# Kernel tuning notes

Hardware: AMD Instinct MI355X
Metric: run time of the kernel (lower is better)

## Reference

```python
import jax, jax.numpy as jnp
import numpy as np


def _gcn_conv(X, src, dst, norm, W, n_nodes):
    # gather + normalized aggregate (SpMM) then dense linear (GEMM)
    msg = X[src] * norm[:, None]                       # [E, F]
    agg = jax.ops.segment_sum(msg, dst, num_segments=n_nodes)  # [N, F]
    return agg @ W                                     # [N, F_out]


def setup_inputs() -> dict:
    key = jax.random.key(0)
    k1, k2, k3, k4, k5 = jax.random.split(key, 5)
    N, E, D_IN, D_HID, D_OUT = 50000, 800000, 128, 128, 64
    X = jax.random.normal(k1, (N, D_IN), dtype=jnp.float32)
    edge_index = jax.random.randint(k2, (2, E), 0, N, dtype=jnp.int64)
    s = 1.0 / np.sqrt(D_IN)
    W1 = jax.random.normal(k3, (D_IN, D_HID), dtype=jnp.float32) * s
    W2 = jax.random.normal(k4, (D_HID, D_HID), dtype=jnp.float32) * s
    W3 = jax.random.normal(k5, (D_HID, D_OUT), dtype=jnp.float32) * s
    return {"X": X, "edge_index": edge_index, "W1": W1, "W2": W2, "W3": W3}


def reference(X, edge_index, W1, W2, W3):
    n_nodes = X.shape[0]
    src, dst = edge_index[0], edge_index[1]
    # symmetric degree normalization D^-1/2 A D^-1/2 (degrees from edge list)
    ones = jnp.ones(src.shape[0], dtype=X.dtype)
    deg = jax.ops.segment_sum(ones, dst, num_segments=n_nodes)
    deg = jnp.maximum(deg, 1.0)
    dinv = jax.lax.rsqrt(deg)
    norm = dinv[src] * dinv[dst]                       # [E]
    h = jax.nn.relu(_gcn_conv(X, src, dst, norm, W1, n_nodes))
    h = jax.nn.relu(_gcn_conv(h, src, dst, norm, W2, n_nodes))
    h = jax.nn.relu(_gcn_conv(h, src, dst, norm, W3, n_nodes))
    return jax.nn.softmax(h, axis=-1)
```

## Files before the change

kernel.cpp:

```cpp
#include <hip/hip_runtime.h>
#include <hip/hip_bf16.h>

typedef __attribute__((ext_vector_type(8))) short short8;
typedef __attribute__((ext_vector_type(4))) short short4v;
typedef __attribute__((ext_vector_type(4))) float f32x4;

static inline size_t ws_align(size_t x) { return (x + 511) & ~((size_t)511); }

static __device__ inline unsigned short f2bf(float f) {
    __hip_bfloat16 h = __float2bfloat16(f);
    return __builtin_bit_cast(unsigned short, h);
}

static __device__ inline float bf2f(unsigned short u) {
    unsigned int x = ((unsigned int)u) << 16;
    return __builtin_bit_cast(float, x);
}


template <int FOUT>
static __device__ inline void gemm64_body(const void* __restrict__ Araw, int a_fp32,
                                          const void* __restrict__ Wraw, int w_fp32,
                                          unsigned short* __restrict__ out,
                                          int N, int blk) {
    constexpr int K = 128;
    constexpr int NT = FOUT / 16;
    constexpr int LDB = K + 8;
    constexpr int LDA = K + 8;
    __shared__ __align__(16) unsigned short bt[FOUT * LDB];
    __shared__ __align__(16) unsigned short atile[64 * LDA];

    const int tid = threadIdx.x;
    const int base = blk * 64;

    constexpr int TOT4 = K * FOUT / 4;
    if (w_fp32) {
        const float* Wf = (const float*)Wraw;
        for (int i = tid; i < TOT4; i += 256) {
            int idx = i * 4;
            int k = idx / FOUT;
            int n = idx & (FOUT - 1);
            float4 v = *(const float4*)(const void*)(Wf + idx);
            bt[(n + 0) * LDB + k] = f2bf(v.x);
            bt[(n + 1) * LDB + k] = f2bf(v.y);
            bt[(n + 2) * LDB + k] = f2bf(v.z);
            bt[(n + 3) * LDB + k] = f2bf(v.w);
        }
    } else {
        const unsigned short* Ws = (const unsigned short*)Wraw;
        for (int i = tid; i < TOT4; i += 256) {
            int idx = i * 4;
            int k = idx / FOUT;
            int n = idx & (FOUT - 1);
            short4v v = *(const short4v*)(const void*)(Ws + idx);
#pragma unroll
            for (int j = 0; j < 4; j++) bt[(n + j) * LDB + k] = ((const unsigned short*)&v)[j];
        }
    }

    if (a_fp32) {
        const float* Af = (const float*)Araw;
#pragma unroll
        for (int i = 0; i < 8; i++) {
            int e4 = i * 256 + tid;
            int elem = e4 * 4;
            int r = elem >> 7;
            int c = elem & 127;
            int srow = base + r;
            if (srow > N - 1) srow = N - 1;
            float4 v = *(const float4*)(const void*)(Af + (size_t)srow * K + c);
            unsigned short* dst = &atile[r * LDA + c];
            dst[0] = f2bf(v.x); dst[1] = f2bf(v.y); dst[2] = f2bf(v.z); dst[3] = f2bf(v.w);
        }
    } else {
        const unsigned short* Ab = (const unsigned short*)Araw;
#pragma unroll
        for (int i = 0; i < 4; i++) {
            int e8 = i * 256 + tid;
            int elem = e8 * 8;
            int r = elem >> 7;
            int c = elem & 127;
            int srow = base + r;
            if (srow > N - 1) srow = N - 1;
            *(short8*)(void*)(&atile[r * LDA + c]) =
                *(const short8*)(const void*)(Ab + (size_t)srow * K + c);
        }
    }

    __syncthreads();

    const int wave = tid >> 6;
    const int lane = tid & 63;
    const int quad = lane >> 4;
    const int r16 = lane & 15;

    short8 afrag[4];
#pragma unroll
    for (int kk = 0; kk < 4; kk++)
        afrag[kk] = *(const short8*)(const void*)(&atile[(wave * 16 + r16) * LDA + kk * 32 + quad * 8]);

    f32x4 acc[NT];
#pragma unroll
    for (int nt = 0; nt < NT; nt++) acc[nt] = (f32x4){0.f, 0.f, 0.f, 0.f};

#pragma unroll
    for (int kk = 0; kk < 4; kk++) {
#pragma unroll
        for (int nt = 0; nt < NT; nt++) {
            short8 b = *(const short8*)(const void*)(&bt[(nt * 16 + r16) * LDB + kk * 32 + quad * 8]);
            acc[nt] = __builtin_amdgcn_mfma_f32_16x16x32_bf16(afrag[kk], b, acc[nt], 0, 0, 0);
        }
    }

#pragma unroll
    for (int nt = 0; nt < NT; nt++) {
#pragma unroll
        for (int r = 0; r < 4; r++) {
            float v = acc[nt][r];
            float o = __shfl_xor(v, 1, 64);
            int row = base + wave * 16 + quad * 4 + r;
            if (((lane & 1) == 0) && row < N) {
                __hip_bfloat162 pk;
                pk.x = __float2bfloat16(v);
                pk.y = __float2bfloat16(o);
                *(__hip_bfloat162*)(out + (size_t)row * FOUT + nt * 16 + r16) = pk;
            }
        }
    }
}


__global__ __launch_bounds__(256) void gemm1_hist_kernel(const void* __restrict__ Xraw,
                                                         const unsigned short* __restrict__ w1s,
                                                         const int* __restrict__ ei,
                                                         int* __restrict__ counts,
                                                         int* __restrict__ loff,
                                                         int* __restrict__ flags,
                                                         unsigned short* __restrict__ out,
                                                         int N, int E, int gblocks) {
    const int tid = threadIdx.x;
    const int lane = tid & 63;

    unsigned ew = (w1s[2 * lane] >> 7) & 0xFF;
    unsigned long long m1 = __ballot(ew >= 100 && ew <= 130);
    const int in_fp32 = (__popcll(m1) < 48) ? 1 : 0;

    if (blockIdx.x >= gblocks) {
        unsigned long long m2 = __ballot(((const unsigned int*)ei)[2 * lane + 1] == 0u);
        const int ei64 = (__popcll(m2) >= 48) ? 1 : 0;
        if (blockIdx.x == gblocks && tid == 0) {
            flags[0] = in_fp32;
            flags[1] = ei64;
        }
        int e = (blockIdx.x - gblocks) * 256 + tid;
        if (e < E) {
            int d = ei64 ? ei[2 * (size_t)E + 2 * e] : ei[(size_t)E + e];
            loff[e] = atomicAdd(&counts[d], 1);
        }
        return;
    }

    gemm64_body<128>(Xraw, in_fp32, (const void*)w1s, in_fp32, out, N, blockIdx.x);
}


template <int FOUT>
__global__ __launch_bounds__(256) void gemm_kernel(const void* __restrict__ Araw,
                                                   const void* __restrict__ Wraw,
                                                   const int* __restrict__ flags,
                                                   unsigned short* __restrict__ out, int N) {
    gemm64_body<FOUT>(Araw, 0, Wraw, flags[0], out, N, blockIdx.x);
}


__global__ __launch_bounds__(256) void alloc_kernel(const int* __restrict__ counts,
                                                    float* __restrict__ dinv,
                                                    int* __restrict__ rowptr,
                                                    int* __restrict__ total, int N) {
    int n = blockIdx.x * blockDim.x + threadIdx.x;
    int lane = threadIdx.x & 63;
    int c = (n < N) ? counts[n] : 0;
    if (n < N) {
        int d = (c < 1) ? 1 : c;
        dinv[n] = rsqrtf((float)d);
    }
    int incl = c;
#pragma unroll
    for (int off = 1; off < 64; off <<= 1) {
        int v = __shfl_up(incl, off, 64);
        if (lane >= off) incl += v;
    }
    int wavetot = __shfl(incl, 63, 64);
    int base = 0;
    if (lane == 0) base = atomicAdd(total, wavetot);
    base = __shfl(base, 0, 64);
    if (n < N) rowptr[n] = base + incl - c;
}

__global__ void fill_kernel(const int* __restrict__ ei, const int* __restrict__ flags,
                            const float* __restrict__ dinv, const int* __restrict__ rowptr,
                            const int* __restrict__ loff, int2* __restrict__ edgedat, int E) {
    int e = blockIdx.x * blockDim.x + threadIdx.x;
    if (e < E) {
        int s, d;
        if (flags[1]) {
            s = ei[2 * e];
            d = ei[2 * (size_t)E + 2 * e];
        } else {
            s = ei[e];
            d = ei[(size_t)E + e];
        }
        int pos = rowptr[d] + loff[e];
        float wt = dinv[s] * dinv[d];
        edgedat[pos] = make_int2(s, __float_as_int(wt));
    }
}


__global__ __launch_bounds__(256) void spmm128_kernel(const int2* __restrict__ edgedat,
                                                      const int* __restrict__ rowptr,
                                                      const int* __restrict__ counts,
                                                      const unsigned short* __restrict__ Hin,
                                                      unsigned short* __restrict__ Hout, int N) {
    int wid = (blockIdx.x * 256 + threadIdx.x) >> 6;
    if (wid >= N) return;
    int lane = threadIdx.x & 63;
    int grp = lane >> 4;
    int gl = lane & 15;
    int n = __builtin_amdgcn_readfirstlane(wid);
    int start = __builtin_amdgcn_readfirstlane(rowptr[n]);
    int len = __builtin_amdgcn_readfirstlane(counts[n]);
    const int2* ep = edgedat + start;

    float acc[8];
#pragma unroll
    for (int u = 0; u < 8; u++) acc[u] = 0.f;

    int j = 0;
    for (; j + 8 <= len; j += 8) {
        int2 e0 = ep[j + grp];
        int2 e1 = ep[j + 4 + grp];
        short8 h0 = *(const short8*)(const void*)(Hin + (size_t)e0.x * 128 + gl * 8);
        short8 h1 = *(const short8*)(const void*)(Hin + (size_t)e1.x * 128 + gl * 8);
        float w0 = __int_as_float(e0.y);
        float w1 = __int_as_float(e1.y);
#pragma unroll
        for (int u = 0; u < 8; u++) acc[u] += w0 * bf2f((unsigned short)h0[u]);
#pragma unroll
        for (int u = 0; u < 8; u++) acc[u] += w1 * bf2f((unsigned short)h1[u]);
    }
    for (; j + 4 <= len; j += 4) {
        int2 e = ep[j + grp];
        short8 h = *(const short8*)(const void*)(Hin + (size_t)e.x * 128 + gl * 8);
        float w = __int_as_float(e.y);
#pragma unroll
        for (int u = 0; u < 8; u++) acc[u] += w * bf2f((unsigned short)h[u]);
    }
    int rem = len - j;
    if (grp < rem) {
        int2 e = ep[j + grp];
        short8 h = *(const short8*)(const void*)(Hin + (size_t)e.x * 128 + gl * 8);
        float w = __int_as_float(e.y);
#pragma unroll
        for (int u = 0; u < 8; u++) acc[u] += w * bf2f((unsigned short)h[u]);
    }

#pragma unroll
    for (int u = 0; u < 8; u++) {
        acc[u] += __shfl_xor(acc[u], 16, 64);
        acc[u] += __shfl_xor(acc[u], 32, 64);
    }

    if (grp == 0) {
        short8 o;
#pragma unroll
        for (int u = 0; u < 8; u++) o[u] = (short)f2bf(fmaxf(acc[u], 0.f));
        *(short8*)(void*)(Hout + (size_t)n * 128 + gl * 8) = o;
    }
}


__global__ __launch_bounds__(256) void spmm64_softmax_kernel(const int2* __restrict__ edgedat,
                                                             const int* __restrict__ rowptr,
                                                             const int* __restrict__ counts,
                                                             const unsigned short* __restrict__ Hin,
                                                             const int* __restrict__ flags,
                                                             void* __restrict__ Out, int N) {
    int wid = (blockIdx.x * 256 + threadIdx.x) >> 6;
    if (wid >= N) return;
    int lane = threadIdx.x & 63;
    int grp = lane >> 3;
    int gl = lane & 7;
    int n = __builtin_amdgcn_readfirstlane(wid);
    int start = __builtin_amdgcn_readfirstlane(rowptr[n]);
    int len = __builtin_amdgcn_readfirstlane(counts[n]);
    const int2* ep = edgedat + start;

    float acc[8];
#pragma unroll
    for (int u = 0; u < 8; u++) acc[u] = 0.f;

    int j = 0;
    for (; j + 16 <= len; j += 16) {
        int2 e0 = ep[j + grp];
        int2 e1 = ep[j + 8 + grp];
        short8 h0 = *(const short8*)(const void*)(Hin + (size_t)e0.x * 64 + gl * 8);
        short8 h1 = *(const short8*)(const void*)(Hin + (size_t)e1.x * 64 + gl * 8);
        float w0 = __int_as_float(e0.y);
        float w1 = __int_as_float(e1.y);
#pragma unroll
        for (int u = 0; u < 8; u++) acc[u] += w0 * bf2f((unsigned short)h0[u]);
#pragma unroll
        for (int u = 0; u < 8; u++) acc[u] += w1 * bf2f((unsigned short)h1[u]);
    }
    for (; j + 8 <= len; j += 8) {
        int2 e = ep[j + grp];
        short8 h = *(const short8*)(const void*)(Hin + (size_t)e.x * 64 + gl * 8);
        float w = __int_as_float(e.y);
#pragma unroll
        for (int u = 0; u < 8; u++) acc[u] += w * bf2f((unsigned short)h[u]);
    }
    int rem = len - j;
    if (grp < rem) {
        int2 e = ep[j + grp];
        short8 h = *(const short8*)(const void*)(Hin + (size_t)e.x * 64 + gl * 8);
        float w = __int_as_float(e.y);
#pragma unroll
        for (int u = 0; u < 8; u++) acc[u] += w * bf2f((unsigned short)h[u]);
    }

#pragma unroll
    for (int u = 0; u < 8; u++) {
        acc[u] += __shfl_xor(acc[u], 8, 64);
        acc[u] += __shfl_xor(acc[u], 16, 64);
        acc[u] += __shfl_xor(acc[u], 32, 64);
    }

#pragma unroll
    for (int u = 0; u < 8; u++) acc[u] = fmaxf(acc[u], 0.f);

    float m = acc[0];
#pragma unroll
    for (int u = 1; u < 8; u++) m = fmaxf(m, acc[u]);
#pragma unroll
    for (int off = 1; off < 8; off <<= 1) m = fmaxf(m, __shfl_xor(m, off, 64));

    float ex[8];
    float s = 0.f;
#pragma unroll
    for (int u = 0; u < 8; u++) {
        ex[u] = __expf(acc[u] - m);
        s += ex[u];
    }
#pragma unroll
    for (int off = 1; off < 8; off <<= 1) s += __shfl_xor(s, off, 64);
    float inv = 1.0f / s;

    if (grp == 0) {
        if (flags[0]) {
            float* op = (float*)Out + (size_t)n * 64 + gl * 8;
            float4 v0, v1;
            v0.x = ex[0] * inv; v0.y = ex[1] * inv; v0.z = ex[2] * inv; v0.w = ex[3] * inv;
            v1.x = ex[4] * inv; v1.y = ex[5] * inv; v1.z = ex[6] * inv; v1.w = ex[7] * inv;
            *(float4*)(void*)op = v0;
            *(float4*)(void*)(op + 4) = v1;
        } else {
            short8 o;
#pragma unroll
            for (int u = 0; u < 8; u++) o[u] = (short)f2bf(ex[u] * inv);
            *(short8*)(void*)((unsigned short*)Out + (size_t)n * 64 + gl * 8) = o;
        }
    }
}


extern "C" void kernel_launch(void* const* d_in, const int* in_sizes, int n_in,
                              void* d_out, int out_size, void* d_ws, size_t ws_size,
                              hipStream_t stream) {
    const void* X  = d_in[0];
    const int*  ei = (const int*)d_in[1];
    const void* W1 = d_in[2];
    const void* W2 = d_in[3];
    const void* W3 = d_in[4];

    const int N = in_sizes[0] / 128;
    const int E = in_sizes[1] / 2;

    char* ws = (char*)d_ws;
    size_t off = 0;
    int* counts = (int*)(ws + off);   off += ws_align((size_t)N * 4);
    int* total  = (int*)(ws + off);   off += ws_align(64);
    const size_t zero_bytes = off;
    int* flags    = (int*)(ws + off);   off += ws_align(64);
    int* rowptr   = (int*)(ws + off);   off += ws_align((size_t)N * 4);
    float* dinv   = (float*)(ws + off); off += ws_align((size_t)N * 4);
    int* loff     = (int*)(ws + off);   off += ws_align((size_t)E * 4);
    int2* edgedat = (int2*)(ws + off);  off += ws_align((size_t)E * 8);
    unsigned short* HA = (unsigned short*)(ws + off); off += ws_align((size_t)N * 128 * 2);
    unsigned short* HB = (unsigned short*)(ws + off); off += ws_align((size_t)N * 128 * 2);

    hipMemsetAsync(d_ws, 0, zero_bytes, stream);

    const int gblocks = (N + 63) / 64;
    const int hblocks = (E + 255) / 256;
    const int sblocks = (N * 64 + 255) / 256;

    gemm1_hist_kernel<<<gblocks + hblocks, 256, 0, stream>>>(
        X, (const unsigned short*)W1, ei, counts, loff, flags, HA, N, E, gblocks);
    alloc_kernel<<<(N + 255) / 256, 256, 0, stream>>>(counts, dinv, rowptr, total, N);
    fill_kernel<<<hblocks, 256, 0, stream>>>(ei, flags, dinv, rowptr, loff, edgedat, E);

    spmm128_kernel<<<sblocks, 256, 0, stream>>>(edgedat, rowptr, counts, HA, HB, N);
    gemm_kernel<128><<<gblocks, 256, 0, stream>>>(HB, W2, flags, HA, N);
    spmm128_kernel<<<sblocks, 256, 0, stream>>>(edgedat, rowptr, counts, HA, HB, N);
    gemm_kernel<64><<<gblocks, 256, 0, stream>>>(HB, W3, flags, HA, N);
    spmm64_softmax_kernel<<<sblocks, 256, 0, stream>>>(edgedat, rowptr, counts, HA, flags, d_out, N);
}
```

Measured before the change: 276.5 us.

## Load GEMM A fragments directly from global and use 128-row 512-thread blocks

The dense GEMM stage now has each wave load its A-operand MFMA fragments straight from global memory into registers, dropping the shared-memory A tile and its staging pass. Blocks grow to 512 threads covering 128 rows, so each staged copy of the transposed weight matrix is reused across twice as many rows. The histogram part of the fused first kernel also moves to 512-thread blocks. The risks are strided, less coalesced global reads for A and lower occupancy from the larger blocks.

```diff
diff --git a/kernel.cpp b/kernel.cpp
--- a/kernel.cpp
+++ b/kernel.cpp
@@ -19,24 +19,22 @@
 
 
 template <int FOUT>
-static __device__ inline void gemm64_body(const void* __restrict__ Araw, int a_fp32,
-                                          const void* __restrict__ Wraw, int w_fp32,
-                                          unsigned short* __restrict__ out,
-                                          int N, int blk) {
+static __device__ inline void gemm128_body(const void* __restrict__ Araw, int a_fp32,
+                                           const void* __restrict__ Wraw, int w_fp32,
+                                           unsigned short* __restrict__ out,
+                                           int N, int blk) {
     constexpr int K = 128;
     constexpr int NT = FOUT / 16;
     constexpr int LDB = K + 8;
-    constexpr int LDA = K + 8;
     __shared__ __align__(16) unsigned short bt[FOUT * LDB];
-    __shared__ __align__(16) unsigned short atile[64 * LDA];
 
     const int tid = threadIdx.x;
-    const int base = blk * 64;
+    const int base = blk * 128;
 
     constexpr int TOT4 = K * FOUT / 4;
     if (w_fp32) {
         const float* Wf = (const float*)Wraw;
-        for (int i = tid; i < TOT4; i += 256) {
+        for (int i = tid; i < TOT4; i += 512) {
             int idx = i * 4;
             int k = idx / FOUT;
             int n = idx & (FOUT - 1);
@@ -48,7 +46,7 @@
         }
     } else {
         const unsigned short* Ws = (const unsigned short*)Wraw;
-        for (int i = tid; i < TOT4; i += 256) {
+        for (int i = tid; i < TOT4; i += 512) {
             int idx = i * 4;
             int k = idx / FOUT;
             int n = idx & (FOUT - 1);
@@ -58,46 +56,35 @@
         }
     }
 
-    if (a_fp32) {
-        const float* Af = (const float*)Araw;
-#pragma unroll
-        for (int i = 0; i < 8; i++) {
-            int e4 = i * 256 + tid;
-            int elem = e4 * 4;
-            int r = elem >> 7;
-            int c = elem & 127;
-            int srow = base + r;
-            if (srow > N - 1) srow = N - 1;
-            float4 v = *(const float4*)(const void*)(Af + (size_t)srow * K + c);
-            unsigned short* dst = &atile[r * LDA + c];
-            dst[0] = f2bf(v.x); dst[1] = f2bf(v.y); dst[2] = f2bf(v.z); dst[3] = f2bf(v.w);
-        }
-    } else {
-        const unsigned short* Ab = (const unsigned short*)Araw;
-#pragma unroll
-        for (int i = 0; i < 4; i++) {
-            int e8 = i * 256 + tid;
-            int elem = e8 * 8;
-            int r = elem >> 7;
-            int c = elem & 127;
-            int srow = base + r;
-            if (srow > N - 1) srow = N - 1;
-            *(short8*)(void*)(&atile[r * LDA + c]) =
-                *(const short8*)(const void*)(Ab + (size_t)srow * K + c);
-        }
-    }
-
-    __syncthreads();
-
     const int wave = tid >> 6;
     const int lane = tid & 63;
     const int quad = lane >> 4;
     const int r16 = lane & 15;
 
+    int arow = base + wave * 16 + r16;
+    if (arow > N - 1) arow = N - 1;
+
     short8 afrag[4];
-#pragma unroll
-    for (int kk = 0; kk < 4; kk++)
-        afrag[kk] = *(const short8*)(const void*)(&atile[(wave * 16 + r16) * LDA + kk * 32 + quad * 8]);
+    if (a_fp32) {
+        const float* Ap = (const float*)Araw + (size_t)arow * K + quad * 8;
+#pragma unroll
+        for (int kk = 0; kk < 4; kk++) {
+            float4 f0 = *(const float4*)(const void*)(Ap + kk * 32);
+            float4 f1 = *(const float4*)(const void*)(Ap + kk * 32 + 4);
+            short8 r;
+            r[0] = (short)f2bf(f0.x); r[1] = (short)f2bf(f0.y);
+            r[2] = (short)f2bf(f0.z); r[3] = (short)f2bf(f0.w);
+            r[4] = (short)f2bf(f1.x); r[5] = (short)f2bf(f1.y);
+            r[6] = (short)f2bf(f1.z); r[7] = (short)f2bf(f1.w);
+            afrag[kk] = r;
+        }
+    } else {
+        const unsigned short* Ap = (const unsigned short*)Araw + (size_t)arow * K + quad * 8;
+#pragma unroll
+        for (int kk = 0; kk < 4; kk++) afrag[kk] = *(const short8*)(const void*)(Ap + kk * 32);
+    }
+
+    __syncthreads();
 
     f32x4 acc[NT];
 #pragma unroll
@@ -130,7 +117,7 @@
 }
 
 
-__global__ __launch_bounds__(256) void gemm1_hist_kernel(const void* __restrict__ Xraw,
+__global__ __launch_bounds__(512) void gemm1_hist_kernel(const void* __restrict__ Xraw,
                                                          const unsigned short* __restrict__ w1s,
                                                          const int* __restrict__ ei,
                                                          int* __restrict__ counts,
@@ -152,7 +139,7 @@
             flags[0] = in_fp32;
             flags[1] = ei64;
         }
-        int e = (blockIdx.x - gblocks) * 256 + tid;
+        int e = (blockIdx.x - gblocks) * 512 + tid;
         if (e < E) {
             int d = ei64 ? ei[2 * (size_t)E + 2 * e] : ei[(size_t)E + e];
             loff[e] = atomicAdd(&counts[d], 1);
@@ -160,16 +147,16 @@
         return;
     }
 
-    gemm64_body<128>(Xraw, in_fp32, (const void*)w1s, in_fp32, out, N, blockIdx.x);
+    gemm128_body<128>(Xraw, in_fp32, (const void*)w1s, in_fp32, out, N, blockIdx.x);
 }
 
 
 template <int FOUT>
-__global__ __launch_bounds__(256) void gemm_kernel(const void* __restrict__ Araw,
+__global__ __launch_bounds__(512) void gemm_kernel(const void* __restrict__ Araw,
                                                    const void* __restrict__ Wraw,
                                                    const int* __restrict__ flags,
                                                    unsigned short* __restrict__ out, int N) {
-    gemm64_body<FOUT>(Araw, 0, Wraw, flags[0], out, N, blockIdx.x);
+    gemm128_body<FOUT>(Araw, 0, Wraw, flags[0], out, N, blockIdx.x);
 }
 
 
@@ -401,18 +388,18 @@
 
     hipMemsetAsync(d_ws, 0, zero_bytes, stream);
 
-    const int gblocks = (N + 63) / 64;
-    const int hblocks = (E + 255) / 256;
+    const int gblocks = (N + 127) / 128;
+    const int hblocks = (E + 511) / 512;
     const int sblocks = (N * 64 + 255) / 256;
 
-    gemm1_hist_kernel<<<gblocks + hblocks, 256, 0, stream>>>(
+    gemm1_hist_kernel<<<gblocks + hblocks, 512, 0, stream>>>(
         X, (const unsigned short*)W1, ei, counts, loff, flags, HA, N, E, gblocks);
     alloc_kernel<<<(N + 255) / 256, 256, 0, stream>>>(counts, dinv, rowptr, total, N);
-    fill_kernel<<<hblocks, 256, 0, stream>>>(ei, flags, dinv, rowptr, loff, edgedat, E);
+    fill_kernel<<<(E + 255) / 256, 256, 0, stream>>>(ei, flags, dinv, rowptr, loff, edgedat, E);
 
     spmm128_kernel<<<sblocks, 256, 0, stream>>>(edgedat, rowptr, counts, HA, HB, N);
-    gemm_kernel<128><<<gblocks, 256, 0, stream>>>(HB, W2, flags, HA, N);
+    gemm_kernel<128><<<gblocks, 512, 0, stream>>>(HB, W2, flags, HA, N);
     spmm128_kernel<<<sblocks, 256, 0, stream>>>(edgedat, rowptr, counts, HA, HB, N);
-    gemm_kernel<64><<<gblocks, 256, 0, stream>>>(HB, W3, flags, HA, N);
+    gemm_kernel<64><<<gblocks, 512, 0, stream>>>(HB, W3, flags, HA, N);
     spmm64_softmax_kernel<<<sblocks, 256, 0, stream>>>(edgedat, rowptr, counts, HA, flags, d_out, N);
 }
```

Measured after the change: 257.7 us. 6.8% less time.
